# Kernel tuning notes

Measured on AMD Instinct MI355X. Metric: run time of the kernel, lower is better.

Reference implementation:

```python
import jax, jax.numpy as jnp
import numpy as np

N_NODES = 50000
N_EDGES = 512000
D = 128          # node_state_dim
H = 256          # edge hidden / message dim = 2*D (GRU input size)


def _edge_mlp(x, W1, b1, W2, b2):
    # Linear -> ReLU -> Linear, matching nn.Sequential built in build_model
    h = jax.nn.relu(x @ W1.T + b1)
    return h @ W2.T + b2


def _prop_once(node_states, f_idx, t_idx, W1, b1, W2, b2):
    # gather endpoints, concat, edge MLP, scatter-add into destination nodes
    edge_in = jnp.concatenate([node_states[f_idx], node_states[t_idx]], axis=-1)  # [E, 2D]
    msgs = _edge_mlp(edge_in, W1, b1, W2, b2)                                     # [E, H]
    return jax.ops.segment_sum(msgs, t_idx, num_segments=N_NODES)                 # [N, H]


def _gru_cell(x, h, W_ih, W_hh, b_ih, b_hh):
    # PyTorch GRU cell convention
    gi = x @ W_ih.T + b_ih   # [N, 3D]
    gh = h @ W_hh.T + b_hh   # [N, 3D]
    ir, iz, inn = jnp.split(gi, 3, axis=-1)
    hr, hz, hn = jnp.split(gh, 3, axis=-1)
    r = jax.nn.sigmoid(ir + hr)
    z = jax.nn.sigmoid(iz + hz)
    n = jnp.tanh(inn + r * hn)
    return (1.0 - z) * n + z * h


def setup_inputs() -> dict:
    key = jax.random.key(0)
    ks = jax.random.split(key, 16)
    s = 0.1  # edge_net_init_scale-ish small init
    inp = {
        "node_states": jax.random.normal(ks[0], (N_NODES, D), dtype=jnp.float32),
        "from_idx": jax.random.randint(ks[1], (N_EDGES,), 0, N_NODES),
        "to_idx": jax.random.randint(ks[2], (N_EDGES,), 0, N_NODES),
        # forward message net: Linear(2D->H), Linear(H->H)
        "Wf1": jax.random.normal(ks[3], (H, 2 * D), dtype=jnp.float32) * s,
        "bf1": jnp.zeros((H,), jnp.float32),
        "Wf2": jax.random.normal(ks[4], (H, H), dtype=jnp.float32) * s,
        "bf2": jnp.zeros((H,), jnp.float32),
        # reverse message net (separate params)
        "Wr1": jax.random.normal(ks[5], (H, 2 * D), dtype=jnp.float32) * s,
        "br1": jnp.zeros((H,), jnp.float32),
        "Wr2": jax.random.normal(ks[6], (H, H), dtype=jnp.float32) * s,
        "br2": jnp.zeros((H,), jnp.float32),
        # GRU(input=2D, hidden=D) params, torch layout
        "W_ih": jax.random.normal(ks[7], (3 * D, 2 * D), dtype=jnp.float32) * 0.05,
        "W_hh": jax.random.normal(ks[8], (3 * D, D), dtype=jnp.float32) * 0.05,
        "b_ih": jnp.zeros((3 * D,), jnp.float32),
        "b_hh": jnp.zeros((3 * D,), jnp.float32),
    }
    return inp


def reference(node_states, from_idx, to_idx, Wf1, bf1, Wf2, bf2,
              Wr1, br1, Wr2, br2, W_ih, W_hh, b_ih, b_hh):
    agg = _prop_once(node_states, from_idx, to_idx, Wf1, bf1, Wf2, bf2)
    agg = agg + _prop_once(node_states, to_idx, from_idx, Wr1, br1, Wr2, br2)
    return _gru_cell(agg, node_states, W_ih, W_hh, b_ih, b_hh)  # [N, D]
```

## Files before the change

kernel.cpp:

```cpp
#include <hip/hip_runtime.h>
#include <stdint.h>


#define NN 50000
#define NE 512000
#define SCAN_N (2 * NN)
#define SCAN_BLOCKS ((SCAN_N + 1023) / 1024)

typedef unsigned short u16;
typedef unsigned int u32;
using h2  = __attribute__((ext_vector_type(2))) _Float16;
using h4  = __attribute__((ext_vector_type(4))) _Float16;
using h8  = __attribute__((ext_vector_type(8))) _Float16;
using f4v = __attribute__((ext_vector_type(4))) float;

__device__ __forceinline__ float h2f(u16 u) {
  _Float16 h; __builtin_memcpy(&h, &u, 2); return (float)h;
}
__device__ __forceinline__ u16 f2h(float f) {
  _Float16 h = (_Float16)f; u16 u; __builtin_memcpy(&u, &h, 2); return u;
}

__global__ __launch_bounds__(256) void k_prep(
    const float* __restrict__ Wf1, const float* __restrict__ bf1,
    const float* __restrict__ Wr1, const float* __restrict__ br1,
    const float* __restrict__ W_ih, const float* __restrict__ Wf2,
    const float* __restrict__ Wr2, const float* __restrict__ W_hh,
    const float* __restrict__ bf2, const float* __restrict__ br2,
    const float* __restrict__ ns,
    const int* __restrict__ from, const int* __restrict__ to,
    u16* __restrict__ Wc16, float* __restrict__ biascat,
    u16* __restrict__ G16, u16* __restrict__ Wh16,
    float* __restrict__ vf, float* __restrict__ vr,
    u16* __restrict__ nsf, int* __restrict__ cnt) {
  const int b = blockIdx.x, tid = threadIdx.x;
  if (b < 512) {
    int c = b * 2 + (tid >> 7);
    int k = tid & 127;
    const float* src;
    if (c < 256)      src = Wf1 + (size_t)c * 256;
    else if (c < 512) src = Wr1 + (size_t)(c - 256) * 256 + 128;
    else if (c < 768) src = Wf1 + (size_t)(c - 512) * 256 + 128;
    else              src = Wr1 + (size_t)(c - 768) * 256;
    float v = src[k];
    int nt = c >> 4, kt = k >> 5, g = (k & 31) >> 3, j = k & 7;
    int lane = (c & 15) + g * 16;
    Wc16[((size_t)nt * 4 + kt) * 512 + lane * 8 + j] = f2h(v);
    if (k == 0) biascat[c] = (c < 256) ? bf1[c] : ((c >= 768) ? br1[c - 768] : 0.f);
  } else if (b < 1280) {
    int bb = b - 512;
    int c = bb % 384, w = bb / 384;
    const float* W2 = w ? Wr2 : Wf2;
    int k = tid;
    float acc = 0.f;
    for (int o = 0; o < 256; ++o)
      acc = fmaf(W_ih[(size_t)c * 256 + o], W2[(size_t)o * 256 + k], acc);
    int kg = w * 256 + k;
    int nt = c >> 4, kt = kg >> 5, g = (kg & 31) >> 3, j = kg & 7;
    int lane = (c & 15) + g * 16;
    G16[((size_t)nt * 16 + kt) * 512 + lane * 8 + j] = f2h(acc);
  } else if (b < 1472) {
    int c = (b - 1280) * 2 + (tid >> 7);
    int k = tid & 127;
    float v = W_hh[(size_t)c * 128 + k];
    int nt = c >> 4, kt = k >> 5, g = (k & 31) >> 3, j = k & 7;
    int lane = (c & 15) + g * 16;
    Wh16[((size_t)nt * 4 + kt) * 512 + lane * 8 + j] = f2h(v);
  } else if (b < 1474) {
    int c = (b - 1472) * 256 + tid;
    if (c < 384) {
      float a = 0.f, bb = 0.f;
      for (int o = 0; o < 256; ++o) {
        float w = W_ih[(size_t)c * 256 + o];
        a = fmaf(w, bf2[o], a);
        bb = fmaf(w, br2[o], bb);
      }
      vf[c] = a; vr[c] = bb;
    }
  } else if (b < 4599) {
    int t = (b - 1474) * 256 + tid;
    int n = t >> 4, kk8 = t & 15;
    float4 v0 = *(const float4*)(ns + (size_t)n * 128 + kk8 * 8);
    float4 v1 = *(const float4*)(ns + (size_t)n * 128 + kk8 * 8 + 4);
    u16 hv[8] = {f2h(v0.x), f2h(v0.y), f2h(v0.z), f2h(v0.w),
                 f2h(v1.x), f2h(v1.y), f2h(v1.z), f2h(v1.w)};
    int mt = n >> 4, r = n & 15, kt = kk8 >> 2, g = kk8 & 3;
    int lane = r + g * 16;
    *(uint4*)(nsf + ((size_t)mt * 4 + kt) * 512 + lane * 8) = *(const uint4*)hv;
  } else {
    int e = (b - 4599) * 256 + tid;
    if (e < NE) {
      atomicAdd(cnt + to[e], 1);
      atomicAdd(cnt + NN + from[e], 1);
    }
  }
}

__global__ __launch_bounds__(256) void k_scanA(const int* __restrict__ cnt,
                                               int* __restrict__ bsum) {
  __shared__ int part[256];
  int b = blockIdx.x, tid = threadIdx.x;
  int idx = b * 1024 + tid * 4;
  int s = 0;
  if (idx + 3 < SCAN_N) {
    int4 v = *(const int4*)(cnt + idx);
    s = v.x + v.y + v.z + v.w;
  } else {
    for (int q = 0; q < 4; ++q)
      if (idx + q < SCAN_N) s += cnt[idx + q];
  }
  part[tid] = s;
  __syncthreads();
  for (int d = 128; d > 0; d >>= 1) {
    if (tid < d) part[tid] += part[tid + d];
    __syncthreads();
  }
  if (tid == 0) bsum[b] = part[0];
}

__global__ __launch_bounds__(256) void k_scanC(const int* __restrict__ cnt,
                                               const int* __restrict__ bsum,
                                               int* __restrict__ off,
                                               int* __restrict__ cur) {
  __shared__ int part[256];
  __shared__ int bs[SCAN_BLOCKS];
  int b = blockIdx.x, tid = threadIdx.x;
  if (tid < SCAN_BLOCKS) bs[tid] = bsum[tid];
  int idx = b * 1024 + tid * 4;
  int c[4] = {0, 0, 0, 0};
  if (idx + 3 < SCAN_N) {
    int4 v = *(const int4*)(cnt + idx);
    c[0] = v.x; c[1] = v.y; c[2] = v.z; c[3] = v.w;
  } else {
    for (int q = 0; q < 4; ++q)
      if (idx + q < SCAN_N) c[q] = cnt[idx + q];
  }
  int s = c[0] + c[1] + c[2] + c[3];
  part[tid] = s;
  __syncthreads();
  for (int d = 1; d < 256; d <<= 1) {
    int x = (tid >= d) ? part[tid - d] : 0;
    __syncthreads();
    part[tid] += x;
    __syncthreads();
  }
  int pre = 0;
  for (int j = 0; j < b; ++j) pre += bs[j];
  int run = pre + ((tid > 0) ? part[tid - 1] : 0);
#pragma unroll
  for (int q = 0; q < 4; ++q) {
    if (idx + q < SCAN_N) {
      off[idx + q] = run;
      cur[idx + q] = run;
      run += c[q];
    }
  }
  if (b == 0 && tid == 0) off[SCAN_N] = 2 * NE;
}

__global__ void k_fill(const int* __restrict__ from, const int* __restrict__ to,
                       int* __restrict__ cur, int* __restrict__ nbr) {
  int e = blockIdx.x * 256 + threadIdx.x;
  if (e < NE) {
    int f = from[e], t = to[e];
    nbr[atomicAdd(cur + t, 1)] = f;
    nbr[atomicAdd(cur + NN + f, 1)] = t;
  }
}

__global__ __launch_bounds__(256) void k_proj(const u16* __restrict__ nsf,
                                              const u16* __restrict__ Wc16,
                                              const float* __restrict__ biascat,
                                              u16* __restrict__ Tin,
                                              u16* __restrict__ Tnode,
                                              u16* __restrict__ Tout) {
  const int w = threadIdx.x >> 6, lane = threadIdx.x & 63;
  const int mt0 = blockIdx.x * 4;
  const int nt0 = blockIdx.y * 16 + w * 4;
  const h8 hzv = {(_Float16)0.f, (_Float16)0.f, (_Float16)0.f, (_Float16)0.f,
                  (_Float16)0.f, (_Float16)0.f, (_Float16)0.f, (_Float16)0.f};
  f4v acc[4][4];
#pragma unroll
  for (int m = 0; m < 4; ++m)
#pragma unroll
    for (int n = 0; n < 4; ++n) acc[m][n] = (f4v){0.f, 0.f, 0.f, 0.f};

#pragma unroll
  for (int kt = 0; kt < 4; ++kt) {
    h8 a[4], b[4];
#pragma unroll
    for (int m = 0; m < 4; ++m) {
      int mt = mt0 + m;
      a[m] = (mt < 3125) ? *(const h8*)(nsf + ((size_t)mt * 4 + kt) * 512 + lane * 8) : hzv;
    }
#pragma unroll
    for (int n = 0; n < 4; ++n)
      b[n] = *(const h8*)(Wc16 + ((size_t)(nt0 + n) * 4 + kt) * 512 + lane * 8);
#pragma unroll
    for (int m = 0; m < 4; ++m)
#pragma unroll
      for (int n = 0; n < 4; ++n)
        acc[m][n] = __builtin_amdgcn_mfma_f32_16x16x32_f16(a[m], b[n], acc[m][n], 0, 0, 0);
  }

  const int c0 = lane & 15, rB = (lane >> 4) * 4;
#pragma unroll
  for (int n = 0; n < 4; ++n) {
    const int ntg = nt0 + n;
    u16* dst;
    size_t stride;
    int col;
    if (ntg < 16)      { dst = Tin;   stride = 256; col = ntg * 16 + c0; }
    else if (ntg < 48) { dst = Tnode; stride = 512; col = (ntg - 16) * 16 + c0; }
    else               { dst = Tout;  stride = 256; col = (ntg - 48) * 16 + c0; }
    float bias = biascat[ntg * 16 + c0];
#pragma unroll
    for (int m = 0; m < 4; ++m) {
      int mt = mt0 + m;
      if (mt >= 3125) continue;
#pragma unroll
      for (int reg = 0; reg < 4; ++reg) {
        int row = mt * 16 + rB + reg;
        dst[(size_t)row * stride + col] = f2h(acc[m][n][reg] + bias);
      }
    }
  }
}

__global__ __launch_bounds__(512) void k_fused(const u16* __restrict__ Tin,
                                               const u16* __restrict__ Tnode,
                                               const u16* __restrict__ Tout,
                                               const int* __restrict__ nbr,
                                               const int* __restrict__ off,
                                               const u16* __restrict__ nsf,
                                               const u16* __restrict__ G16,
                                               const u16* __restrict__ Wh16,
                                               const float* __restrict__ ns,
                                               const float* __restrict__ b_ih,
                                               const float* __restrict__ b_hh,
                                               const float* __restrict__ vf,
                                               const float* __restrict__ vr,
                                               float* __restrict__ out) {
  __shared__ __align__(16) u16 sfl[2 * 16 * 512];
  __shared__ int ctr;
  const int wid = threadIdx.x >> 6, lane = threadIdx.x & 63;
  const int mt0 = blockIdx.x * 2;
  const bool has1 = (mt0 + 1) < 3125;
  const h2 z2 = {(_Float16)0.f, (_Float16)0.f};

  if (threadIdx.x == 0) ctr = 0;
  __syncthreads();

  const int g = (lane & 7) >> 1, j0 = (lane & 1) * 4;
#define LOADF(q_, kbase_) \
  (*(const h4*)(gtab + (size_t)__builtin_amdgcn_readlane(nb, (kbase_) + (q_)) * 256 + lane * 4))
#define CONSUME(wvq_)                                           \
  {                                                             \
    h2 t01 = {(wvq_)[0], (wvq_)[1]};                            \
    h2 t23 = {(wvq_)[2], (wvq_)[3]};                            \
    t01 = __builtin_elementwise_max(t01 + inv01, z2);           \
    t23 = __builtin_elementwise_max(t23 + inv23, z2);           \
    a0 += (float)t01[0]; a1 += (float)t01[1];                   \
    a2 += (float)t23[0]; a3 += (float)t23[1];                   \
  }
  for (;;) {
    int t0 = 0;
    if (lane == 0) t0 = atomicAdd(&ctr, 1);
    const int task = __shfl(t0, 0);
    if (task >= 64) break;
    const int nn = task >> 1, dir = task & 1;
    const int n = mt0 * 16 + nn;
    if (n >= NN) continue;
    const u16* gtab = dir ? Tout : Tin;
    const int invofs = dir ? 0 : 256;
    h4 invv = __builtin_nontemporal_load(
        (const h4*)(Tnode + (size_t)n * 512 + invofs + lane * 4));
    h2 inv01 = {invv[0], invv[1]};
    h2 inv23 = {invv[2], invv[3]};
    const int s = off[dir * NN + n];
    const int e = off[dir * NN + n + 1];
    float a0 = 0.f, a1 = 0.f, a2 = 0.f, a3 = 0.f;
    for (int i = s; i < e; i += 64) {
      int nb = (i + lane < e) ? __builtin_nontemporal_load(nbr + i + lane) : 0;
      int cnt = min(64, e - i);
      int k = 0;
      for (; k + 7 < cnt; k += 8) {
        h4 w0 = LOADF(0, k), w1 = LOADF(1, k), w2 = LOADF(2, k), w3 = LOADF(3, k);
        h4 w4 = LOADF(4, k), w5 = LOADF(5, k), w6 = LOADF(6, k), w7 = LOADF(7, k);
        CONSUME(w0) CONSUME(w1) CONSUME(w2) CONSUME(w3)
        CONSUME(w4) CONSUME(w5) CONSUME(w6) CONSUME(w7)
      }
      if (k + 3 < cnt) {
        h4 w0 = LOADF(0, k), w1 = LOADF(1, k), w2 = LOADF(2, k), w3 = LOADF(3, k);
        CONSUME(w0) CONSUME(w1) CONSUME(w2) CONSUME(w3)
        k += 4;
      }
      for (; k < cnt; ++k) {
        h4 w0 = LOADF(0, k);
        CONSUME(w0)
      }
    }
    const int m = nn >> 4, r = nn & 15;
    const int kt = dir * 8 + (lane >> 3);
    const int laneF = r + g * 16;
    const int slot = laneF ^ (lane >> 3);
    u16 hv[4] = {f2h(a0), f2h(a1), f2h(a2), f2h(a3)};
    *(ushort4*)(sfl + ((m * 16 + kt) * 512) + slot * 8 + j0) = *(const ushort4*)hv;
  }
#undef LOADF
#undef CONSUME

  const int base = wid;
  const h8 hz = {(_Float16)0.f, (_Float16)0.f, (_Float16)0.f, (_Float16)0.f,
                 (_Float16)0.f, (_Float16)0.f, (_Float16)0.f, (_Float16)0.f};
  f4v gh[2][3], gi[2][3];
#pragma unroll
  for (int m = 0; m < 2; ++m)
#pragma unroll
    for (int gg = 0; gg < 3; ++gg) {
      gh[m][gg] = (f4v){0.f, 0.f, 0.f, 0.f};
      gi[m][gg] = (f4v){0.f, 0.f, 0.f, 0.f};
    }
#pragma unroll
  for (int kt = 0; kt < 4; ++kt) {
    h8 a0 = *(const h8*)(nsf + ((size_t)mt0 * 4 + kt) * 512 + lane * 8);
    h8 a1 = has1 ? *(const h8*)(nsf + ((size_t)(mt0 + 1) * 4 + kt) * 512 + lane * 8) : hz;
#pragma unroll
    for (int gg = 0; gg < 3; ++gg) {
      h8 b = *(const h8*)(Wh16 + ((size_t)(base + 8 * gg) * 4 + kt) * 512 + lane * 8);
      gh[0][gg] = __builtin_amdgcn_mfma_f32_16x16x32_f16(a0, b, gh[0][gg], 0, 0, 0);
      gh[1][gg] = __builtin_amdgcn_mfma_f32_16x16x32_f16(a1, b, gh[1][gg], 0, 0, 0);
    }
  }

  __syncthreads();

#pragma unroll
  for (int kt = 0; kt < 16; ++kt) {
    const int slot = lane ^ (kt & 7);
    h8 a0 = *(const h8*)(sfl + (0 * 16 + kt) * 512 + slot * 8);
    h8 a1 = has1 ? *(const h8*)(sfl + (1 * 16 + kt) * 512 + slot * 8) : hz;
#pragma unroll
    for (int gg = 0; gg < 3; ++gg) {
      h8 b = *(const h8*)(G16 + ((size_t)(base + 8 * gg) * 16 + kt) * 512 + lane * 8);
      gi[0][gg] = __builtin_amdgcn_mfma_f32_16x16x32_f16(a0, b, gi[0][gg], 0, 0, 0);
      gi[1][gg] = __builtin_amdgcn_mfma_f32_16x16x32_f16(a1, b, gi[1][gg], 0, 0, 0);
    }
  }

  const int c0 = lane & 15, rB = (lane >> 4) * 4;
  const int d = base * 16 + c0;
  const float vf0 = vf[d], vf1 = vf[128 + d], vf2 = vf[256 + d];
  const float vr0 = vr[d], vr1 = vr[128 + d], vr2 = vr[256 + d];
  const float bi0 = b_ih[d], bi1 = b_ih[128 + d], bi2 = b_ih[256 + d];
  const float bh0 = b_hh[d], bh1 = b_hh[128 + d], bh2 = b_hh[256 + d];
#pragma unroll
  for (int m = 0; m < 2; ++m) {
    if (m == 1 && !has1) continue;
    const int mt = mt0 + m;
#pragma unroll
    for (int reg = 0; reg < 4; ++reg) {
      int row = mt * 16 + rB + reg;
      float idg = (float)(off[row + 1] - off[row]);
      float odg = (float)(off[NN + row + 1] - off[NN + row]);
      float gr = gi[m][0][reg] + idg * vf0 + odg * vr0 + bi0;
      float gz = gi[m][1][reg] + idg * vf1 + odg * vr1 + bi1;
      float gn = gi[m][2][reg] + idg * vf2 + odg * vr2 + bi2;
      float hr = gh[m][0][reg] + bh0;
      float hzv = gh[m][1][reg] + bh1;
      float hn = gh[m][2][reg] + bh2;
      float rg = 1.f / (1.f + __expf(-(gr + hr)));
      float zg = 1.f / (1.f + __expf(-(gz + hzv)));
      float ng = tanhf(gn + rg * hn);
      float h = ns[(size_t)row * 128 + d];
      out[(size_t)row * 128 + d] = (1.f - zg) * ng + zg * h;
    }
  }
}

extern "C" void kernel_launch(void* const* d_in, const int* in_sizes, int n_in,
                              void* d_out, int out_size, void* d_ws, size_t ws_size,
                              hipStream_t stream) {
  const float* ns   = (const float*)d_in[0];
  const int* from   = (const int*)d_in[1];
  const int* to     = (const int*)d_in[2];
  const float* Wf1  = (const float*)d_in[3];
  const float* bf1  = (const float*)d_in[4];
  const float* Wf2  = (const float*)d_in[5];
  const float* bf2  = (const float*)d_in[6];
  const float* Wr1  = (const float*)d_in[7];
  const float* br1  = (const float*)d_in[8];
  const float* Wr2  = (const float*)d_in[9];
  const float* br2  = (const float*)d_in[10];
  const float* W_ih = (const float*)d_in[11];
  const float* W_hh = (const float*)d_in[12];
  const float* b_ih = (const float*)d_in[13];
  const float* b_hh = (const float*)d_in[14];
  float* out = (float*)d_out;

  char* w = (char*)d_ws;
  u16*   Wc16    = (u16*)(w + 0);
  float* biascat = (float*)(w + 262144);
  u16*   G16     = (u16*)(w + 266240);
  u16*   Wh16    = (u16*)(w + 659456);
  float* vf      = (float*)(w + 757760);
  float* vr      = (float*)(w + 759296);
  int*   cnt     = (int*)(w + 760832);
  int*   off     = (int*)(w + 1160960);
  int*   cur     = (int*)(w + 1561088);
  int*   bsum    = (int*)(w + 1961216);
  int*   nbr     = (int*)(w + 1961728);
  u16*   nsf     = (u16*)(w + 6057728);
  u16*   Tin     = (u16*)(w + 18857728);
  u16*   Tout    = (u16*)(w + 44457728);
  u16*   Tnode   = (u16*)(w + 70057728);

  hipMemsetAsync(cnt, 0, 400000, stream);

  k_prep<<<6599, 256, 0, stream>>>(Wf1, bf1, Wr1, br1, W_ih, Wf2, Wr2, W_hh,
                                   bf2, br2, ns, from, to, Wc16, biascat, G16,
                                   Wh16, vf, vr, nsf, cnt);

  k_scanA<<<SCAN_BLOCKS, 256, 0, stream>>>(cnt, bsum);
  k_scanC<<<SCAN_BLOCKS, 256, 0, stream>>>(cnt, bsum, off, cur);
  k_fill<<<(NE + 255) / 256, 256, 0, stream>>>(from, to, cur, nbr);

  k_proj<<<dim3(782, 4), 256, 0, stream>>>(nsf, Wc16, biascat, Tin, Tnode, Tout);
  k_fused<<<1563, 512, 0, stream>>>(Tin, Tnode, Tout, nbr, off, nsf, G16, Wh16,
                                    ns, b_ih, b_hh, vf, vr, out);
}
```

Baseline: 346.4 us.

## Merge CSR fill into projection kernel and make fused kernel persistent

The edge-fill kernel and the node projection GEMM now run as one launch, with the first 2000 blocks doing the atomic CSR fill and the rest doing the MFMA projection. This removes a launch and lets the two independent phases overlap. The fused aggregation/GRU kernel becomes persistent: 1024 blocks pull tile indices from a global atomic counter that is zeroed by the existing memset. This cuts tail effects and block launch overhead, at the cost of an extra block-wide barrier per tile and a fixed grid size.

```diff
diff --git a/kernel.cpp b/kernel.cpp
--- a/kernel.cpp
+++ b/kernel.cpp
@@ -6,6 +6,7 @@
 #define NE 512000
 #define SCAN_N (2 * NN)
 #define SCAN_BLOCKS ((SCAN_N + 1023) / 1024)
+#define NTILES 1563
 
 typedef unsigned short u16;
 typedef unsigned int u32;
@@ -158,25 +159,27 @@
   if (b == 0 && tid == 0) off[SCAN_N] = 2 * NE;
 }
 
-__global__ void k_fill(const int* __restrict__ from, const int* __restrict__ to,
-                       int* __restrict__ cur, int* __restrict__ nbr) {
-  int e = blockIdx.x * 256 + threadIdx.x;
-  if (e < NE) {
-    int f = from[e], t = to[e];
-    nbr[atomicAdd(cur + t, 1)] = f;
-    nbr[atomicAdd(cur + NN + f, 1)] = t;
-  }
-}
-
-__global__ __launch_bounds__(256) void k_proj(const u16* __restrict__ nsf,
-                                              const u16* __restrict__ Wc16,
-                                              const float* __restrict__ biascat,
-                                              u16* __restrict__ Tin,
-                                              u16* __restrict__ Tnode,
-                                              u16* __restrict__ Tout) {
+__global__ __launch_bounds__(256) void k_projfill(
+    const u16* __restrict__ nsf, const u16* __restrict__ Wc16,
+    const float* __restrict__ biascat,
+    u16* __restrict__ Tin, u16* __restrict__ Tnode, u16* __restrict__ Tout,
+    const int* __restrict__ from, const int* __restrict__ to,
+    int* __restrict__ cur, int* __restrict__ nbr) {
+  const int b = blockIdx.x;
+  if (b < 2000) {
+    int e = b * 256 + threadIdx.x;
+    if (e < NE) {
+      int f = from[e], t = to[e];
+      nbr[atomicAdd(cur + t, 1)] = f;
+      nbr[atomicAdd(cur + NN + f, 1)] = t;
+    }
+    return;
+  }
+  const int bb = b - 2000;
+  const int bx = bb % 782, by = bb / 782;
   const int w = threadIdx.x >> 6, lane = threadIdx.x & 63;
-  const int mt0 = blockIdx.x * 4;
-  const int nt0 = blockIdx.y * 16 + w * 4;
+  const int mt0 = bx * 4;
+  const int nt0 = by * 16 + w * 4;
   const h8 hzv = {(_Float16)0.f, (_Float16)0.f, (_Float16)0.f, (_Float16)0.f,
                   (_Float16)0.f, (_Float16)0.f, (_Float16)0.f, (_Float16)0.f};
   f4v acc[4][4];
@@ -187,7 +190,7 @@
 
 #pragma unroll
   for (int kt = 0; kt < 4; ++kt) {
-    h8 a[4], b[4];
+    h8 a[4], bfr[4];
 #pragma unroll
     for (int m = 0; m < 4; ++m) {
       int mt = mt0 + m;
@@ -195,12 +198,12 @@
     }
 #pragma unroll
     for (int n = 0; n < 4; ++n)
-      b[n] = *(const h8*)(Wc16 + ((size_t)(nt0 + n) * 4 + kt) * 512 + lane * 8);
+      bfr[n] = *(const h8*)(Wc16 + ((size_t)(nt0 + n) * 4 + kt) * 512 + lane * 8);
 #pragma unroll
     for (int m = 0; m < 4; ++m)
 #pragma unroll
       for (int n = 0; n < 4; ++n)
-        acc[m][n] = __builtin_amdgcn_mfma_f32_16x16x32_f16(a[m], b[n], acc[m][n], 0, 0, 0);
+        acc[m][n] = __builtin_amdgcn_mfma_f32_16x16x32_f16(a[m], bfr[n], acc[m][n], 0, 0, 0);
   }
 
   const int c0 = lane & 15, rB = (lane >> 4) * 4;
@@ -240,18 +243,28 @@
                                                const float* __restrict__ b_hh,
                                                const float* __restrict__ vf,
                                                const float* __restrict__ vr,
+                                               int* __restrict__ gctr,
                                                float* __restrict__ out) {
   __shared__ __align__(16) u16 sfl[2 * 16 * 512];
   __shared__ int ctr;
+  __shared__ int tile_s;
   const int wid = threadIdx.x >> 6, lane = threadIdx.x & 63;
-  const int mt0 = blockIdx.x * 2;
-  const bool has1 = (mt0 + 1) < 3125;
   const h2 z2 = {(_Float16)0.f, (_Float16)0.f};
-
-  if (threadIdx.x == 0) ctr = 0;
-  __syncthreads();
-
   const int g = (lane & 7) >> 1, j0 = (lane & 1) * 4;
+  const h8 hz = {(_Float16)0.f, (_Float16)0.f, (_Float16)0.f, (_Float16)0.f,
+                 (_Float16)0.f, (_Float16)0.f, (_Float16)0.f, (_Float16)0.f};
+
+  for (;;) {
+    if (threadIdx.x == 0) {
+      tile_s = atomicAdd(gctr, 1);
+      ctr = 0;
+    }
+    __syncthreads();
+    const int tile = tile_s;
+    if (tile >= NTILES) break;
+    const int mt0 = tile * 2;
+    const bool has1 = (mt0 + 1) < 3125;
+
 #define LOADF(q_, kbase_) \
   (*(const h4*)(gtab + (size_t)__builtin_amdgcn_readlane(nb, (kbase_) + (q_)) * 256 + lane * 4))
 #define CONSUME(wvq_)                                           \
@@ -263,118 +276,119 @@
     a0 += (float)t01[0]; a1 += (float)t01[1];                   \
     a2 += (float)t23[0]; a3 += (float)t23[1];                   \
   }
-  for (;;) {
-    int t0 = 0;
-    if (lane == 0) t0 = atomicAdd(&ctr, 1);
-    const int task = __shfl(t0, 0);
-    if (task >= 64) break;
-    const int nn = task >> 1, dir = task & 1;
-    const int n = mt0 * 16 + nn;
-    if (n >= NN) continue;
-    const u16* gtab = dir ? Tout : Tin;
-    const int invofs = dir ? 0 : 256;
-    h4 invv = __builtin_nontemporal_load(
-        (const h4*)(Tnode + (size_t)n * 512 + invofs + lane * 4));
-    h2 inv01 = {invv[0], invv[1]};
-    h2 inv23 = {invv[2], invv[3]};
-    const int s = off[dir * NN + n];
-    const int e = off[dir * NN + n + 1];
-    float a0 = 0.f, a1 = 0.f, a2 = 0.f, a3 = 0.f;
-    for (int i = s; i < e; i += 64) {
-      int nb = (i + lane < e) ? __builtin_nontemporal_load(nbr + i + lane) : 0;
-      int cnt = min(64, e - i);
-      int k = 0;
-      for (; k + 7 < cnt; k += 8) {
-        h4 w0 = LOADF(0, k), w1 = LOADF(1, k), w2 = LOADF(2, k), w3 = LOADF(3, k);
-        h4 w4 = LOADF(4, k), w5 = LOADF(5, k), w6 = LOADF(6, k), w7 = LOADF(7, k);
-        CONSUME(w0) CONSUME(w1) CONSUME(w2) CONSUME(w3)
-        CONSUME(w4) CONSUME(w5) CONSUME(w6) CONSUME(w7)
-      }
-      if (k + 3 < cnt) {
-        h4 w0 = LOADF(0, k), w1 = LOADF(1, k), w2 = LOADF(2, k), w3 = LOADF(3, k);
-        CONSUME(w0) CONSUME(w1) CONSUME(w2) CONSUME(w3)
-        k += 4;
-      }
-      for (; k < cnt; ++k) {
-        h4 w0 = LOADF(0, k);
-        CONSUME(w0)
-      }
-    }
-    const int m = nn >> 4, r = nn & 15;
-    const int kt = dir * 8 + (lane >> 3);
-    const int laneF = r + g * 16;
-    const int slot = laneF ^ (lane >> 3);
-    u16 hv[4] = {f2h(a0), f2h(a1), f2h(a2), f2h(a3)};
-    *(ushort4*)(sfl + ((m * 16 + kt) * 512) + slot * 8 + j0) = *(const ushort4*)hv;
-  }
+    for (;;) {
+      int t0 = 0;
+      if (lane == 0) t0 = atomicAdd(&ctr, 1);
+      const int task = __shfl(t0, 0);
+      if (task >= 64) break;
+      const int nn = task >> 1, dir = task & 1;
+      const int n = mt0 * 16 + nn;
+      if (n >= NN) continue;
+      const u16* gtab = dir ? Tout : Tin;
+      const int invofs = dir ? 0 : 256;
+      h4 invv = __builtin_nontemporal_load(
+          (const h4*)(Tnode + (size_t)n * 512 + invofs + lane * 4));
+      h2 inv01 = {invv[0], invv[1]};
+      h2 inv23 = {invv[2], invv[3]};
+      const int s = off[dir * NN + n];
+      const int e = off[dir * NN + n + 1];
+      float a0 = 0.f, a1 = 0.f, a2 = 0.f, a3 = 0.f;
+      for (int i = s; i < e; i += 64) {
+        int nb = (i + lane < e) ? __builtin_nontemporal_load(nbr + i + lane) : 0;
+        int cnt = min(64, e - i);
+        int k = 0;
+        for (; k + 7 < cnt; k += 8) {
+          h4 w0 = LOADF(0, k), w1 = LOADF(1, k), w2 = LOADF(2, k), w3 = LOADF(3, k);
+          h4 w4 = LOADF(4, k), w5 = LOADF(5, k), w6 = LOADF(6, k), w7 = LOADF(7, k);
+          CONSUME(w0) CONSUME(w1) CONSUME(w2) CONSUME(w3)
+          CONSUME(w4) CONSUME(w5) CONSUME(w6) CONSUME(w7)
+        }
+        if (k + 3 < cnt) {
+          h4 w0 = LOADF(0, k), w1 = LOADF(1, k), w2 = LOADF(2, k), w3 = LOADF(3, k);
+          CONSUME(w0) CONSUME(w1) CONSUME(w2) CONSUME(w3)
+          k += 4;
+        }
+        for (; k < cnt; ++k) {
+          h4 w0 = LOADF(0, k);
+          CONSUME(w0)
+        }
+      }
+      const int m = nn >> 4, r = nn & 15;
+      const int kt = dir * 8 + (lane >> 3);
+      const int laneF = r + g * 16;
+      const int slot = laneF ^ (lane >> 3);
+      u16 hv[4] = {f2h(a0), f2h(a1), f2h(a2), f2h(a3)};
+      *(ushort4*)(sfl + ((m * 16 + kt) * 512) + slot * 8 + j0) = *(const ushort4*)hv;
+    }
 #undef LOADF
 #undef CONSUME
 
-  const int base = wid;
-  const h8 hz = {(_Float16)0.f, (_Float16)0.f, (_Float16)0.f, (_Float16)0.f,
-                 (_Float16)0.f, (_Float16)0.f, (_Float16)0.f, (_Float16)0.f};
-  f4v gh[2][3], gi[2][3];
-#pragma unroll
-  for (int m = 0; m < 2; ++m)
-#pragma unroll
-    for (int gg = 0; gg < 3; ++gg) {
-      gh[m][gg] = (f4v){0.f, 0.f, 0.f, 0.f};
-      gi[m][gg] = (f4v){0.f, 0.f, 0.f, 0.f};
-    }
-#pragma unroll
-  for (int kt = 0; kt < 4; ++kt) {
-    h8 a0 = *(const h8*)(nsf + ((size_t)mt0 * 4 + kt) * 512 + lane * 8);
-    h8 a1 = has1 ? *(const h8*)(nsf + ((size_t)(mt0 + 1) * 4 + kt) * 512 + lane * 8) : hz;
-#pragma unroll
-    for (int gg = 0; gg < 3; ++gg) {
-      h8 b = *(const h8*)(Wh16 + ((size_t)(base + 8 * gg) * 4 + kt) * 512 + lane * 8);
-      gh[0][gg] = __builtin_amdgcn_mfma_f32_16x16x32_f16(a0, b, gh[0][gg], 0, 0, 0);
-      gh[1][gg] = __builtin_amdgcn_mfma_f32_16x16x32_f16(a1, b, gh[1][gg], 0, 0, 0);
-    }
-  }
-
-  __syncthreads();
-
-#pragma unroll
-  for (int kt = 0; kt < 16; ++kt) {
-    const int slot = lane ^ (kt & 7);
-    h8 a0 = *(const h8*)(sfl + (0 * 16 + kt) * 512 + slot * 8);
-    h8 a1 = has1 ? *(const h8*)(sfl + (1 * 16 + kt) * 512 + slot * 8) : hz;
-#pragma unroll
-    for (int gg = 0; gg < 3; ++gg) {
-      h8 b = *(const h8*)(G16 + ((size_t)(base + 8 * gg) * 16 + kt) * 512 + lane * 8);
-      gi[0][gg] = __builtin_amdgcn_mfma_f32_16x16x32_f16(a0, b, gi[0][gg], 0, 0, 0);
-      gi[1][gg] = __builtin_amdgcn_mfma_f32_16x16x32_f16(a1, b, gi[1][gg], 0, 0, 0);
-    }
-  }
-
-  const int c0 = lane & 15, rB = (lane >> 4) * 4;
-  const int d = base * 16 + c0;
-  const float vf0 = vf[d], vf1 = vf[128 + d], vf2 = vf[256 + d];
-  const float vr0 = vr[d], vr1 = vr[128 + d], vr2 = vr[256 + d];
-  const float bi0 = b_ih[d], bi1 = b_ih[128 + d], bi2 = b_ih[256 + d];
-  const float bh0 = b_hh[d], bh1 = b_hh[128 + d], bh2 = b_hh[256 + d];
-#pragma unroll
-  for (int m = 0; m < 2; ++m) {
-    if (m == 1 && !has1) continue;
-    const int mt = mt0 + m;
-#pragma unroll
-    for (int reg = 0; reg < 4; ++reg) {
-      int row = mt * 16 + rB + reg;
-      float idg = (float)(off[row + 1] - off[row]);
-      float odg = (float)(off[NN + row + 1] - off[NN + row]);
-      float gr = gi[m][0][reg] + idg * vf0 + odg * vr0 + bi0;
-      float gz = gi[m][1][reg] + idg * vf1 + odg * vr1 + bi1;
-      float gn = gi[m][2][reg] + idg * vf2 + odg * vr2 + bi2;
-      float hr = gh[m][0][reg] + bh0;
-      float hzv = gh[m][1][reg] + bh1;
-      float hn = gh[m][2][reg] + bh2;
-      float rg = 1.f / (1.f + __expf(-(gr + hr)));
-      float zg = 1.f / (1.f + __expf(-(gz + hzv)));
-      float ng = tanhf(gn + rg * hn);
-      float h = ns[(size_t)row * 128 + d];
-      out[(size_t)row * 128 + d] = (1.f - zg) * ng + zg * h;
-    }
+    const int base = wid;
+    f4v gh[2][3], gi[2][3];
+#pragma unroll
+    for (int m = 0; m < 2; ++m)
+#pragma unroll
+      for (int gg = 0; gg < 3; ++gg) {
+        gh[m][gg] = (f4v){0.f, 0.f, 0.f, 0.f};
+        gi[m][gg] = (f4v){0.f, 0.f, 0.f, 0.f};
+      }
+#pragma unroll
+    for (int kt = 0; kt < 4; ++kt) {
+      h8 a0 = *(const h8*)(nsf + ((size_t)mt0 * 4 + kt) * 512 + lane * 8);
+      h8 a1 = has1 ? *(const h8*)(nsf + ((size_t)(mt0 + 1) * 4 + kt) * 512 + lane * 8) : hz;
+#pragma unroll
+      for (int gg = 0; gg < 3; ++gg) {
+        h8 b = *(const h8*)(Wh16 + ((size_t)(base + 8 * gg) * 4 + kt) * 512 + lane * 8);
+        gh[0][gg] = __builtin_amdgcn_mfma_f32_16x16x32_f16(a0, b, gh[0][gg], 0, 0, 0);
+        gh[1][gg] = __builtin_amdgcn_mfma_f32_16x16x32_f16(a1, b, gh[1][gg], 0, 0, 0);
+      }
+    }
+
+    __syncthreads();
+
+#pragma unroll
+    for (int kt = 0; kt < 16; ++kt) {
+      const int slot = lane ^ (kt & 7);
+      h8 a0 = *(const h8*)(sfl + (0 * 16 + kt) * 512 + slot * 8);
+      h8 a1 = has1 ? *(const h8*)(sfl + (1 * 16 + kt) * 512 + slot * 8) : hz;
+#pragma unroll
+      for (int gg = 0; gg < 3; ++gg) {
+        h8 b = *(const h8*)(G16 + ((size_t)(base + 8 * gg) * 16 + kt) * 512 + lane * 8);
+        gi[0][gg] = __builtin_amdgcn_mfma_f32_16x16x32_f16(a0, b, gi[0][gg], 0, 0, 0);
+        gi[1][gg] = __builtin_amdgcn_mfma_f32_16x16x32_f16(a1, b, gi[1][gg], 0, 0, 0);
+      }
+    }
+
+    const int c0 = lane & 15, rB = (lane >> 4) * 4;
+    const int d = base * 16 + c0;
+    const float vf0 = vf[d], vf1 = vf[128 + d], vf2 = vf[256 + d];
+    const float vr0 = vr[d], vr1 = vr[128 + d], vr2 = vr[256 + d];
+    const float bi0 = b_ih[d], bi1 = b_ih[128 + d], bi2 = b_ih[256 + d];
+    const float bh0 = b_hh[d], bh1 = b_hh[128 + d], bh2 = b_hh[256 + d];
+#pragma unroll
+    for (int m = 0; m < 2; ++m) {
+      if (m == 1 && !has1) continue;
+      const int mt = mt0 + m;
+#pragma unroll
+      for (int reg = 0; reg < 4; ++reg) {
+        int row = mt * 16 + rB + reg;
+        float idg = (float)(off[row + 1] - off[row]);
+        float odg = (float)(off[NN + row + 1] - off[NN + row]);
+        float gr = gi[m][0][reg] + idg * vf0 + odg * vr0 + bi0;
+        float gz = gi[m][1][reg] + idg * vf1 + odg * vr1 + bi1;
+        float gn = gi[m][2][reg] + idg * vf2 + odg * vr2 + bi2;
+        float hr = gh[m][0][reg] + bh0;
+        float hzv = gh[m][1][reg] + bh1;
+        float hn = gh[m][2][reg] + bh2;
+        float rg = 1.f / (1.f + __expf(-(gr + hr)));
+        float zg = 1.f / (1.f + __expf(-(gz + hzv)));
+        float ng = tanhf(gn + rg * hn);
+        float h = ns[(size_t)row * 128 + d];
+        out[(size_t)row * 128 + d] = (1.f - zg) * ng + zg * h;
+      }
+    }
+
+    __syncthreads();
   }
 }
 
@@ -405,17 +419,18 @@
   u16*   Wh16    = (u16*)(w + 659456);
   float* vf      = (float*)(w + 757760);
   float* vr      = (float*)(w + 759296);
-  int*   cnt     = (int*)(w + 760832);
-  int*   off     = (int*)(w + 1160960);
-  int*   cur     = (int*)(w + 1561088);
-  int*   bsum    = (int*)(w + 1961216);
-  int*   nbr     = (int*)(w + 1961728);
-  u16*   nsf     = (u16*)(w + 6057728);
-  u16*   Tin     = (u16*)(w + 18857728);
-  u16*   Tout    = (u16*)(w + 44457728);
-  u16*   Tnode   = (u16*)(w + 70057728);
-
-  hipMemsetAsync(cnt, 0, 400000, stream);
+  int*   gctr    = (int*)(w + 760832);
+  int*   cnt     = (int*)(w + 761088);
+  int*   off     = (int*)(w + 1161216);
+  int*   cur     = (int*)(w + 1561344);
+  int*   bsum    = (int*)(w + 1961472);
+  int*   nbr     = (int*)(w + 1961984);
+  u16*   nsf     = (u16*)(w + 6057984);
+  u16*   Tin     = (u16*)(w + 18857984);
+  u16*   Tout    = (u16*)(w + 44457984);
+  u16*   Tnode   = (u16*)(w + 70057984);
+
+  hipMemsetAsync(w + 760832, 0, 256 + 400000, stream);
 
   k_prep<<<6599, 256, 0, stream>>>(Wf1, bf1, Wr1, br1, W_ih, Wf2, Wr2, W_hh,
                                    bf2, br2, ns, from, to, Wc16, biascat, G16,
@@ -423,9 +438,10 @@
 
   k_scanA<<<SCAN_BLOCKS, 256, 0, stream>>>(cnt, bsum);
   k_scanC<<<SCAN_BLOCKS, 256, 0, stream>>>(cnt, bsum, off, cur);
-  k_fill<<<(NE + 255) / 256, 256, 0, stream>>>(from, to, cur, nbr);
-
-  k_proj<<<dim3(782, 4), 256, 0, stream>>>(nsf, Wc16, biascat, Tin, Tnode, Tout);
-  k_fused<<<1563, 512, 0, stream>>>(Tin, Tnode, Tout, nbr, off, nsf, G16, Wh16,
-                                    ns, b_ih, b_hh, vf, vr, out);
-}
+
+  k_projfill<<<5128, 256, 0, stream>>>(nsf, Wc16, biascat, Tin, Tnode, Tout,
+                                       from, to, cur, nbr);
+
+  k_fused<<<1024, 512, 0, stream>>>(Tin, Tnode, Tout, nbr, off, nsf, G16, Wh16,
+                                    ns, b_ih, b_hh, vf, vr, gctr, out);
+}
```

New measurement: 404.9 us. 1.17x slower.
